# Kernel optimization log

Measured on AMD Instinct MI355X. Metric: run time of the kernel, lower is better.

## Reference

```python
import jax, jax.numpy as jnp
import numpy as np

DIM = 240; NH = 6; HD = 20          # dim, num_heads, head_dim = dim // (2*num_heads)
WS = 16; BWS = 8                    # window size, base window size
R = (WS // BWS) ** 2                # spatial_linear in_features (=4)
LW = WS * WS; LB = BWS * BWS

# static relative-position index for a WSxWS window (same construction as torch buffer)
_coords = np.stack(np.meshgrid(np.arange(WS), np.arange(WS), indexing='ij')).reshape(2, -1)
_rel = (_coords[:, :, None] - _coords[:, None, :]).transpose(1, 2, 0).astype(np.int64)
_rel[..., 0] += WS - 1; _rel[..., 1] += WS - 1; _rel[..., 0] *= 2 * WS - 1
RPI = jnp.asarray(_rel.sum(-1))     # [LW, LW]


def conv2d(x, w, b, pad):
    y = jax.lax.conv_general_dilated(x, w, (1, 1), [(pad, pad), (pad, pad)],
                                     dimension_numbers=('NCHW', 'OIHW', 'NCHW'))
    return y + b[None, :, None, None]


def lrelu(x):
    return jnp.where(x >= 0, x, 0.2 * x)  # LeakyReLU(0.2)


def layer_norm(x, g, b, eps=1e-5):
    m = x.mean(-1, keepdims=True)
    v = jnp.mean((x - m) ** 2, axis=-1, keepdims=True)
    return (x - m) * jax.lax.rsqrt(v + eps) * g + b


def setup_inputs() -> dict:
    key = jax.random.key(0)
    ks = iter(jax.random.split(key, 40))
    rn = lambda shape: jax.random.normal(next(ks), shape, jnp.float32) * 0.02
    B, H, W = 2, 256, 256
    pd = (DIM // 4) // 4  # DynamicPosBias pos_dim = 15
    return {
        'x': jax.random.normal(next(ks), (B, H * W, DIM), jnp.float32),
        # DFE (qv projection)
        'c1_w': rn((DIM // 5, DIM, 1, 1)), 'c1_b': jnp.zeros((DIM // 5,), jnp.float32),
        'c2_w': rn((DIM // 5, DIM // 5, 3, 3)), 'c2_b': jnp.zeros((DIM // 5,), jnp.float32),
        'c3_w': rn((DIM, DIM // 5, 1, 1)), 'c3_b': jnp.zeros((DIM,), jnp.float32),
        'lin_w': rn((DIM, DIM, 1, 1)), 'lin_b': jnp.zeros((DIM,), jnp.float32),
        # spatial linear projection Linear(R, 1)
        'sl_w': rn((1, R)), 'sl_b': jnp.zeros((1,), jnp.float32),
        # DynamicPosBias MLP (residual=False)
        'pp_w': rn((pd, 2)), 'pp_b': jnp.zeros((pd,), jnp.float32),
        'ln1_g': jnp.ones((pd,), jnp.float32), 'ln1_b': jnp.zeros((pd,), jnp.float32),
        'p1_w': rn((pd, pd)), 'p1_b': jnp.zeros((pd,), jnp.float32),
        'ln2_g': jnp.ones((pd,), jnp.float32), 'ln2_b': jnp.zeros((pd,), jnp.float32),
        'p2_w': rn((pd, pd)), 'p2_b': jnp.zeros((pd,), jnp.float32),
        'ln3_g': jnp.ones((pd,), jnp.float32), 'ln3_b': jnp.zeros((pd,), jnp.float32),
        'p3_w': rn((NH, pd)), 'p3_b': jnp.zeros((NH,), jnp.float32),
        # output projection
        'proj_w': rn((DIM, DIM)), 'proj_b': jnp.zeros((DIM,), jnp.float32),
        'H': 256, 'W': 256,
    }


def reference(x, c1_w, c1_b, c2_w, c2_b, c3_w, c3_b, lin_w, lin_b, sl_w, sl_b,
              pp_w, pp_b, ln1_g, ln1_b, p1_w, p1_b, ln2_g, ln2_b, p2_w, p2_b,
              ln3_g, ln3_b, p3_w, p3_b, proj_w, proj_b, H, W):
    B, L, C = x.shape
    # ---- DFE feature projection (conv-gated) ----
    xi = jnp.transpose(x, (0, 2, 1)).reshape(B, C, H, W)
    conv = conv2d(lrelu(conv2d(lrelu(conv2d(xi, c1_w, c1_b, 0)), c2_w, c2_b, 1)), c3_w, c3_b, 0)
    qv = conv * conv2d(xi, lin_w, lin_b, 0)                       # [B,C,H,W]
    qv = jnp.transpose(qv, (0, 2, 3, 1))                          # [B,H,W,C]
    # ---- window partition ----
    nh_w, nw_w = H // WS, W // WS
    qv = qv.reshape(B, nh_w, WS, nw_w, WS, C).transpose(0, 1, 3, 2, 4, 5).reshape(-1, LW, C)
    B_ = qv.shape[0]
    qv = qv.reshape(B_, LW, 2, NH, HD).transpose(2, 0, 3, 1, 4)   # [2,B_,NH,LW,HD]
    q, v = qv[0], qv[1]
    # ---- spatial self-correlation ----
    # spatial linear projection of v: [B_,NH,LW,HD] -> [B_,NH,LB,HD]
    vs = v.reshape(B_, NH, BWS, WS // BWS, BWS, WS // BWS, HD)
    vs = vs.transpose(0, 1, 2, 4, 6, 3, 5).reshape(B_, NH, LB, HD, R)
    vs = jnp.einsum('bnkcr,or->bnkc', vs, sl_w) + sl_b            # Linear(R,1), squeezed
    corr = jnp.einsum('bnlc,bnkc->bnlk', q, vs) / HD              # [B_,NH,LW,LB]
    # dynamic relative position bias (MLP over the mother set of relative coords)
    ph = jnp.arange(1 - WS, WS)
    biases = jnp.stack(jnp.meshgrid(ph, ph, indexing='ij')).reshape(2, -1).T.astype(x.dtype)
    pos = biases @ pp_w.T + pp_b
    pos = jax.nn.relu(layer_norm(pos, ln1_g, ln1_b)) @ p1_w.T + p1_b
    pos = jax.nn.relu(layer_norm(pos, ln2_g, ln2_b)) @ p2_w.T + p2_b
    pos = jax.nn.relu(layer_norm(pos, ln3_g, ln3_b)) @ p3_w.T + p3_b  # [(2*WS-1)^2, NH]
    rpb = jnp.take(pos, RPI.reshape(-1), axis=0).reshape(LW, LW, NH).transpose(2, 0, 1)
    # pool key axis to base-window resolution (consistent with spatial_linear_projection grouping)
    rpb = rpb.reshape(NH, LW, BWS, WS // BWS, BWS, WS // BWS).mean((3, 5)).reshape(NH, LW, LB)
    corr = corr + rpb[None]
    x_s = jnp.einsum('bnlk,bnkc->bnlc', corr, vs)
    x_s = x_s.transpose(0, 2, 1, 3).reshape(B_, LW, NH * HD)      # [B_,LW,C/2]
    # ---- channel self-correlation (single-head over merged channels) ----
    qc = q.transpose(0, 2, 1, 3).reshape(B_, LW, NH * HD)
    vc = v.transpose(0, 2, 1, 3).reshape(B_, LW, NH * HD)
    corr_c = jnp.einsum('blc,bld->bcd', qc, vc) / LW              # [B_,C/2,C/2]
    x_c = jnp.einsum('bcd,bld->blc', corr_c, vc)                  # [B_,LW,C/2]
    # ---- window reverse + spatial-channel fusion ----
    def wrev(t):
        return t.reshape(B, nh_w, nw_w, WS, WS, -1).transpose(0, 1, 3, 2, 4, 5).reshape(B, H, W, -1)
    out = jnp.concatenate([wrev(x_s), wrev(x_c)], axis=-1)        # [B,H,W,C]
    out = out @ proj_w.T + proj_b
    return out.reshape(B, L, C)
```

## Files before the change

### kernel.cpp

```cpp
#include <hip/hip_runtime.h>
#include <math.h>

#define NPIX 131072

typedef __attribute__((ext_vector_type(8))) short bfrag;
typedef __attribute__((ext_vector_type(4))) float facc;
typedef __attribute__((ext_vector_type(4))) unsigned short us4;

__device__ __forceinline__ float lrelu_f(float x) { return x >= 0.f ? x : 0.2f * x; }

__device__ __forceinline__ int pix_of(int w, int l) {
    int b = w >> 8, wi = (w >> 4) & 15, wj = w & 15;
    return ((((b << 4) + wi) * 16 + (l >> 4)) << 8) + (wj << 4) + (l & 15);
}

__device__ __forceinline__ unsigned short bf16rn(float f) {
    unsigned u = __builtin_bit_cast(unsigned, f);
    u += 0x7FFFu + ((u >> 16) & 1u);
    return (unsigned short)(u >> 16);
}
__device__ __forceinline__ float bf16tof(unsigned short h) {
    unsigned u = ((unsigned)h) << 16;
    return __builtin_bit_cast(float, u);
}

__device__ __forceinline__ void split_x_body(const float* __restrict__ x,
                                             unsigned short* __restrict__ xs2, int idx)
{
    int row = idx >> 5;
    int k = (idx & 31) * 8;
    float v[8];
    if (k < 240) {
        float4 a = *(const float4*)(x + (size_t)row * 240 + k);
        float4 b = *(const float4*)(x + (size_t)row * 240 + k + 4);
        v[0] = a.x; v[1] = a.y; v[2] = a.z; v[3] = a.w;
        v[4] = b.x; v[5] = b.y; v[6] = b.z; v[7] = b.w;
    } else {
#pragma unroll
        for (int e = 0; e < 8; ++e) v[e] = 0.f;
    }
    bfrag hi, lo;
#pragma unroll
    for (int e = 0; e < 8; ++e) {
        unsigned short h = bf16rn(v[e]);
        hi[e] = (short)h;
        lo[e] = (short)bf16rn(v[e] - bf16tof(h));
    }
    unsigned short* dst = xs2 + (size_t)row * 512 + k;
    *(bfrag*)(dst) = hi;
    *(bfrag*)(dst + 256) = lo;
}

__device__ __forceinline__ void pack_w_body(const float* __restrict__ src,
                                            int rows, int K,
                                            unsigned short* __restrict__ dst,
                                            int total8, int KPAD, int idx)
{
    if (idx >= total8) return;
    int kper = KPAD >> 3;
    int row = idx / kper;
    int k = (idx - row * kper) * 8;
    float v[8];
#pragma unroll
    for (int e = 0; e < 8; ++e) {
        int kk = k + e;
        v[e] = (row < rows && kk < K) ? src[(size_t)row * K + kk] : 0.f;
    }
    bfrag hi, lo;
#pragma unroll
    for (int e = 0; e < 8; ++e) {
        unsigned short h = bf16rn(v[e]);
        hi[e] = (short)h;
        lo[e] = (short)bf16rn(v[e] - bf16tof(h));
    }
    unsigned short* d = dst + (size_t)row * 2 * KPAD + k;
    *(bfrag*)(d) = hi;
    *(bfrag*)(d + KPAD) = lo;
}

__device__ __forceinline__ void pack_c2w_body(const float* __restrict__ c2_w,
                                              unsigned short* __restrict__ c2w2, int idx)
{
    if (idx >= 6912) return;
    int rowid = idx >> 4;
    int c = idx & 15;
    int tap = rowid / 48, n = rowid - tap * 48;
    int ty = tap / 3, tx = tap - ty * 3;
    int lohalf = c >> 3;
    int cbase = (c & 7) * 8;
    bfrag outv;
#pragma unroll
    for (int e = 0; e < 8; ++e) {
        int ci = cbase + e;
        float v = (ci < 48) ? c2_w[(((size_t)n * 48 + ci) * 3 + ty) * 3 + tx] : 0.f;
        unsigned short h = bf16rn(v);
        outv[e] = (short)(lohalf ? bf16rn(v - bf16tof(h)) : h);
    }
    *(bfrag*)(c2w2 + (size_t)rowid * 128 + c * 8) = outv;
}

__global__ __launch_bounds__(256) void pack_all_kernel(
    const float* __restrict__ lin_w, const float* __restrict__ proj_w,
    const float* __restrict__ c3_w, const float* __restrict__ c1_w,
    const float* __restrict__ c2_w, const float* __restrict__ x,
    unsigned short* __restrict__ lin_w2, unsigned short* __restrict__ proj_w2,
    unsigned short* __restrict__ c3_w2, unsigned short* __restrict__ c1_w2,
    unsigned short* __restrict__ c2w2, unsigned short* __restrict__ xs2)
{
    int blk = blockIdx.x, tid = threadIdx.x;
    if (blk < 32)       pack_w_body(lin_w, 240, 240, lin_w2, 8192, 256, blk * 256 + tid);
    else if (blk < 64)  pack_w_body(proj_w, 240, 240, proj_w2, 8192, 256, (blk - 32) * 256 + tid);
    else if (blk < 72)  pack_w_body(c3_w, 240, 48, c3_w2, 2048, 64, (blk - 64) * 256 + tid);
    else if (blk < 88)  pack_w_body(c1_w, 48, 240, c1_w2, 4096, 256, (blk - 72) * 256 + tid);
    else if (blk < 115) pack_c2w_body(c2_w, c2w2, (blk - 88) * 256 + tid);
    else                split_x_body(x, xs2, (blk - 115) * 256 + tid);
}

__device__ __forceinline__ void ln_relu15(const float* h, float* r,
                                          const float* __restrict__ g,
                                          const float* __restrict__ b) {
    float m = 0.f;
#pragma unroll
    for (int f = 0; f < 15; ++f) m += h[f];
    m *= (1.f / 15.f);
    float v = 0.f;
#pragma unroll
    for (int f = 0; f < 15; ++f) { float d = h[f] - m; v += d * d; }
    float rs = rsqrtf(v * (1.f / 15.f) + 1e-5f);
#pragma unroll
    for (int f = 0; f < 15; ++f) {
        float xx = (h[f] - m) * rs * g[f] + b[f];
        r[f] = xx > 0.f ? xx : 0.f;
    }
}

__device__ __forceinline__ void lin15(const float* r, float* h,
                                      const float* __restrict__ w,
                                      const float* __restrict__ b) {
#pragma unroll
    for (int o = 0; o < 15; ++o) {
        float s = b[o];
#pragma unroll
        for (int g = 0; g < 15; ++g) s += r[g] * w[o * 15 + g];
        h[o] = s;
    }
}

__global__ __launch_bounds__(256) void prep_pos_kernel(
    const float* __restrict__ pp_w, const float* __restrict__ pp_b,
    const float* __restrict__ ln1_g, const float* __restrict__ ln1_b,
    const float* __restrict__ p1_w, const float* __restrict__ p1_b,
    const float* __restrict__ ln2_g, const float* __restrict__ ln2_b,
    const float* __restrict__ p2_w, const float* __restrict__ p2_b,
    const float* __restrict__ ln3_g, const float* __restrict__ ln3_b,
    const float* __restrict__ p3_w, const float* __restrict__ p3_b,
    float* __restrict__ pos3)
{
    int idx = blockIdx.x * 256 + threadIdx.x;
    if (idx >= 961) return;
    float h[15], r[15];
    float in0 = (float)(idx / 31) - 15.f;
    float in1 = (float)(idx % 31) - 15.f;
#pragma unroll
    for (int f = 0; f < 15; ++f) h[f] = in0 * pp_w[2 * f] + in1 * pp_w[2 * f + 1] + pp_b[f];
    ln_relu15(h, r, ln1_g, ln1_b);
    lin15(r, h, p1_w, p1_b);
    ln_relu15(h, r, ln2_g, ln2_b);
    lin15(r, h, p2_w, p2_b);
    ln_relu15(h, r, ln3_g, ln3_b);
#pragma unroll
    for (int o = 0; o < 6; ++o) {
        float s = p3_b[o];
#pragma unroll
        for (int g = 0; g < 15; ++g) s += r[g] * p3_w[o * 15 + g];
        pos3[idx * 6 + o] = s;
    }
}

__global__ __launch_bounds__(256) void rpb_kernel(const float* __restrict__ pos3,
                                                  float* __restrict__ rpb_t)
{
    int out = blockIdx.x * 256 + threadIdx.x;
    int n = out >> 14;
    int k = (out >> 8) & 63;
    int l = out & 255;
    int a = k >> 3, c = k & 7;
    int i1 = l >> 4, j1 = l & 15;
    float s = 0.f;
#pragma unroll
    for (int bb = 0; bb < 2; ++bb)
#pragma unroll
        for (int d = 0; d < 2; ++d) {
            int i2 = a * 2 + bb, j2 = c * 2 + d;
            int rpi = (i1 - i2 + 15) * 31 + (j1 - j2 + 15);
            s += pos3[rpi * 6 + n];
        }
    rpb_t[out] = s * 0.25f;
}

__device__ __forceinline__ void mfma_kpass3(const unsigned short* __restrict__ A2, int lda2,
                                            const unsigned short* __restrict__ W2, int ldw2,
                                            int ksteps, int mbase, int nbase,
                                            short* lds_a, short* lds_w,
                                            int tid, int wm, int wn,
                                            facc acc[4][4])
{
    int lane = tid & 63;
    int i = lane & 15, g = lane >> 4;
    int kpa = lda2 >> 1, kpw = ldw2 >> 1;
    for (int s = 0; s < ksteps; ++s) {
        int k0 = s * 32;
        {
            int r = tid >> 1, h16 = (tid & 1) * 16;
            const unsigned short* src = A2 + (size_t)(mbase + r) * lda2 + k0 + h16;
            bfrag h0 = *(const bfrag*)(src);
            bfrag h1 = *(const bfrag*)(src + 8);
            bfrag l0 = *(const bfrag*)(src + kpa);
            bfrag l1 = *(const bfrag*)(src + kpa + 8);
            short* dst = lds_a + r * 72 + h16;
            *(bfrag*)(dst)      = h0;  *(bfrag*)(dst + 8)  = h1;
            *(bfrag*)(dst + 32) = l0;  *(bfrag*)(dst + 40) = l1;
        }
        {
            int r = tid >> 1, half = tid & 1;
            const unsigned short* src = W2 + (size_t)(nbase + r) * ldw2 + half * kpw + k0;
            bfrag v0 = *(const bfrag*)(src);
            bfrag v1 = *(const bfrag*)(src + 8);
            bfrag v2 = *(const bfrag*)(src + 16);
            bfrag v3 = *(const bfrag*)(src + 24);
            short* dst = lds_w + r * 72 + half * 32;
            *(bfrag*)(dst)      = v0;  *(bfrag*)(dst + 8)  = v1;
            *(bfrag*)(dst + 16) = v2;  *(bfrag*)(dst + 24) = v3;
        }
        __syncthreads();
        bfrag ah[4], al[4], bh[4], bl[4];
#pragma unroll
        for (int mu = 0; mu < 4; ++mu) {
            const short* p = lds_a + (wm * 64 + mu * 16 + i) * 72 + g * 8;
            ah[mu] = *(const bfrag*)(p);
            al[mu] = *(const bfrag*)(p + 32);
        }
#pragma unroll
        for (int nu = 0; nu < 4; ++nu) {
            const short* p = lds_w + (wn * 64 + nu * 16 + i) * 72 + g * 8;
            bh[nu] = *(const bfrag*)(p);
            bl[nu] = *(const bfrag*)(p + 32);
        }
#pragma unroll
        for (int mu = 0; mu < 4; ++mu)
#pragma unroll
            for (int nu = 0; nu < 4; ++nu) {
                acc[mu][nu] = __builtin_amdgcn_mfma_f32_16x16x32_bf16(ah[mu], bh[nu], acc[mu][nu], 0, 0, 0);
                acc[mu][nu] = __builtin_amdgcn_mfma_f32_16x16x32_bf16(ah[mu], bl[nu], acc[mu][nu], 0, 0, 0);
                acc[mu][nu] = __builtin_amdgcn_mfma_f32_16x16x32_bf16(al[mu], bh[nu], acc[mu][nu], 0, 0, 0);
            }
        __syncthreads();
    }
}

__device__ __forceinline__ void mfma_kpass_n64(const unsigned short* __restrict__ A2, int lda2,
                                               const unsigned short* __restrict__ W2, int ldw2,
                                               int ksteps, int mbase,
                                               short* lds_a, short* lds_w,
                                               int tid, int wm, int wn,
                                               facc acc[4][2])
{
    int lane = tid & 63;
    int i = lane & 15, g = lane >> 4;
    int kpa = lda2 >> 1, kpw = ldw2 >> 1;
    for (int s = 0; s < ksteps; ++s) {
        int k0 = s * 32;
        {
            int r = tid >> 1, h16 = (tid & 1) * 16;
            const unsigned short* src = A2 + (size_t)(mbase + r) * lda2 + k0 + h16;
            bfrag h0 = *(const bfrag*)(src);
            bfrag h1 = *(const bfrag*)(src + 8);
            bfrag l0 = *(const bfrag*)(src + kpa);
            bfrag l1 = *(const bfrag*)(src + kpa + 8);
            short* dst = lds_a + r * 72 + h16;
            *(bfrag*)(dst)      = h0;  *(bfrag*)(dst + 8)  = h1;
            *(bfrag*)(dst + 32) = l0;  *(bfrag*)(dst + 40) = l1;
        }
        if (tid < 128) {
            int r = tid >> 1, half = tid & 1;
            const unsigned short* src = W2 + (size_t)r * ldw2 + half * kpw + k0;
            bfrag v0 = *(const bfrag*)(src);
            bfrag v1 = *(const bfrag*)(src + 8);
            bfrag v2 = *(const bfrag*)(src + 16);
            bfrag v3 = *(const bfrag*)(src + 24);
            short* dst = lds_w + r * 72 + half * 32;
            *(bfrag*)(dst)      = v0;  *(bfrag*)(dst + 8)  = v1;
            *(bfrag*)(dst + 16) = v2;  *(bfrag*)(dst + 24) = v3;
        }
        __syncthreads();
        bfrag ah[4], al[4], bh[2], bl[2];
#pragma unroll
        for (int mu = 0; mu < 4; ++mu) {
            const short* p = lds_a + (wm * 64 + mu * 16 + i) * 72 + g * 8;
            ah[mu] = *(const bfrag*)(p);
            al[mu] = *(const bfrag*)(p + 32);
        }
#pragma unroll
        for (int nu = 0; nu < 2; ++nu) {
            const short* p = lds_w + (wn * 32 + nu * 16 + i) * 72 + g * 8;
            bh[nu] = *(const bfrag*)(p);
            bl[nu] = *(const bfrag*)(p + 32);
        }
#pragma unroll
        for (int mu = 0; mu < 4; ++mu)
#pragma unroll
            for (int nu = 0; nu < 2; ++nu) {
                acc[mu][nu] = __builtin_amdgcn_mfma_f32_16x16x32_bf16(ah[mu], bh[nu], acc[mu][nu], 0, 0, 0);
                acc[mu][nu] = __builtin_amdgcn_mfma_f32_16x16x32_bf16(ah[mu], bl[nu], acc[mu][nu], 0, 0, 0);
                acc[mu][nu] = __builtin_amdgcn_mfma_f32_16x16x32_bf16(al[mu], bh[nu], acc[mu][nu], 0, 0, 0);
            }
        __syncthreads();
    }
}

__global__ __launch_bounds__(256, 3) void conv1_mfma_kernel(const unsigned short* __restrict__ xs2,
    const unsigned short* __restrict__ c1_w2, const float* __restrict__ bias,
    unsigned short* __restrict__ t1s)
{
    __shared__ __align__(16) short lds_a[128 * 72];
    __shared__ __align__(16) short lds_w[64 * 72];
    int tid = threadIdx.x;
    int lane = tid & 63, wid = tid >> 6;
    int wm = wid >> 1, wn = wid & 1;
    int mbase = blockIdx.x * 128;
    facc zero = {0.f, 0.f, 0.f, 0.f};
    facc acc[4][2];
#pragma unroll
    for (int mu = 0; mu < 4; ++mu)
#pragma unroll
        for (int nu = 0; nu < 2; ++nu) acc[mu][nu] = zero;

    mfma_kpass_n64(xs2, 512, c1_w2, 512, 8, mbase, lds_a, lds_w, tid, wm, wn, acc);

    int i = lane & 15, g = lane >> 4;
#pragma unroll
    for (int nu = 0; nu < 2; ++nu) {
        int n = wn * 32 + nu * 16 + i;
        if (n < 48) {
            float bv = bias[n];
#pragma unroll
            for (int mu = 0; mu < 4; ++mu)
#pragma unroll
                for (int rr = 0; rr < 4; ++rr) {
                    size_t m = (size_t)mbase + wm * 64 + mu * 16 + g * 4 + rr;
                    float v = lrelu_f(acc[mu][nu][rr] + bv);
                    unsigned short h = bf16rn(v);
                    t1s[m * 128 + n] = h;
                    t1s[m * 128 + 64 + n] = bf16rn(v - bf16tof(h));
                }
        }
    }
    if (tid < 128) {
        size_t m = (size_t)mbase + tid;
        bfrag z = {0, 0, 0, 0, 0, 0, 0, 0};
        *(bfrag*)(t1s + m * 128 + 48)  = z;
        *(bfrag*)(t1s + m * 128 + 56)  = z;
        *(bfrag*)(t1s + m * 128 + 112) = z;
        *(bfrag*)(t1s + m * 128 + 120) = z;
    }
}

__global__ __launch_bounds__(256) void conv2_mfma_kernel(const unsigned short* __restrict__ t1s,
    const unsigned short* __restrict__ c2w2, const float* __restrict__ bias,
    unsigned short* __restrict__ t2s)
{
    __shared__ __align__(16) short a_s[130 * 128];
    int bid = blockIdx.x;
    int xcd = bid & 7;
    int j = bid >> 3;
    int half = j & 1;
    int rl = (j >> 1) & 31;
    int b = j >> 6;
    int r = xcd * 32 + rl;
    int c0 = half * 128;
    int tid = threadIdx.x;
    int lane = tid & 63, wid = tid >> 6;
    int i = lane & 15, g = lane >> 4;
    facc zero = {0.f, 0.f, 0.f, 0.f};
    facc acc[2][3];
#pragma unroll
    for (int mu = 0; mu < 2; ++mu)
#pragma unroll
        for (int nu = 0; nu < 3; ++nu) acc[mu][nu] = zero;

    for (int dy = 0; dy < 3; ++dy) {
        int grow = r + dy - 1;
        bool rowok = (grow >= 0 && grow < 256);
        for (int idx = tid; idx < 130 * 16; idx += 256) {
            int j2 = idx >> 4, ch = idx & 15;
            int gc = c0 - 1 + j2;
            bfrag v = {0, 0, 0, 0, 0, 0, 0, 0};
            if (rowok && gc >= 0 && gc < 256) {
                size_t gpix = ((size_t)b * 256 + grow) * 256 + gc;
                v = *(const bfrag*)(t1s + gpix * 128 + ch * 8);
            }
            *(bfrag*)&a_s[j2 * 128 + ((ch ^ (j2 & 7)) * 8)] = v;
        }
        __syncthreads();
#pragma unroll
        for (int dx = 0; dx < 3; ++dx) {
            const unsigned short* wb = c2w2 + (size_t)(dy * 3 + dx) * 48 * 128;
#pragma unroll
            for (int h = 0; h < 2; ++h) {
                bfrag ah[2], al[2], bh[3], bl[3];
#pragma unroll
                for (int mu = 0; mu < 2; ++mu) {
                    int j2 = wid * 32 + mu * 16 + i + dx;
                    int chi = (h * 4 + g) ^ (j2 & 7);
                    int clo = (8 + h * 4 + g) ^ (j2 & 7);
                    ah[mu] = *(const bfrag*)&a_s[j2 * 128 + chi * 8];
                    al[mu] = *(const bfrag*)&a_s[j2 * 128 + clo * 8];
                }
#pragma unroll
                for (int nu = 0; nu < 3; ++nu) {
                    const unsigned short* wp = wb + (size_t)(nu * 16 + i) * 128 + h * 32 + g * 8;
                    bh[nu] = *(const bfrag*)(wp);
                    bl[nu] = *(const bfrag*)(wp + 64);
                }
#pragma unroll
                for (int mu = 0; mu < 2; ++mu)
#pragma unroll
                    for (int nu = 0; nu < 3; ++nu) {
                        acc[mu][nu] = __builtin_amdgcn_mfma_f32_16x16x32_bf16(ah[mu], bh[nu], acc[mu][nu], 0, 0, 0);
                        acc[mu][nu] = __builtin_amdgcn_mfma_f32_16x16x32_bf16(ah[mu], bl[nu], acc[mu][nu], 0, 0, 0);
                        acc[mu][nu] = __builtin_amdgcn_mfma_f32_16x16x32_bf16(al[mu], bh[nu], acc[mu][nu], 0, 0, 0);
                    }
            }
        }
        __syncthreads();
    }
#pragma unroll
    for (int nu = 0; nu < 3; ++nu) {
        int n = nu * 16 + i;
        float bv = bias[n];
#pragma unroll
        for (int mu = 0; mu < 2; ++mu)
#pragma unroll
            for (int rr = 0; rr < 4; ++rr) {
                int lp = wid * 32 + mu * 16 + g * 4 + rr;
                size_t gpix = ((size_t)b * 256 + r) * 256 + (c0 + lp);
                float v = lrelu_f(acc[mu][nu][rr] + bv);
                unsigned short h = bf16rn(v);
                t2s[gpix * 128 + n] = h;
                t2s[gpix * 128 + 64 + n] = bf16rn(v - bf16tof(h));
            }
    }
    if (tid < 128) {
        size_t gpix = ((size_t)b * 256 + r) * 256 + (c0 + tid);
        bfrag z = {0, 0, 0, 0, 0, 0, 0, 0};
        *(bfrag*)(t2s + gpix * 128 + 48)  = z;
        *(bfrag*)(t2s + gpix * 128 + 56)  = z;
        *(bfrag*)(t2s + gpix * 128 + 112) = z;
        *(bfrag*)(t2s + gpix * 128 + 120) = z;
    }
}

__global__ __launch_bounds__(256) void qv_mfma_kernel(const unsigned short* __restrict__ xs2,
    const unsigned short* __restrict__ lin_w2, const float* __restrict__ lin_b,
    const unsigned short* __restrict__ t2s, const unsigned short* __restrict__ c3_w2,
    const float* __restrict__ c3_b, float* __restrict__ qv)
{
    __shared__ __align__(16) short lds_a[128 * 72];
    __shared__ __align__(16) short lds_w[128 * 72];
    int tid = threadIdx.x;
    int lane = tid & 63, wid = tid >> 6;
    int wm = wid >> 1, wn = wid & 1;
    int bid = blockIdx.y * 2 + blockIdx.x;
    int xcd = bid & 7, j = bid >> 3;
    int mbase = (xcd * 128 + (j >> 1)) * 128;
    int nbase = (j & 1) * 128;
    facc zero = {0.f, 0.f, 0.f, 0.f};
    facc acc1[4][4], acc2[4][4];
#pragma unroll
    for (int mu = 0; mu < 4; ++mu)
#pragma unroll
        for (int nu = 0; nu < 4; ++nu) { acc1[mu][nu] = zero; acc2[mu][nu] = zero; }

    mfma_kpass3(xs2, 512, lin_w2, 512, 8, mbase, nbase, lds_a, lds_w, tid, wm, wn, acc1);
    mfma_kpass3(t2s, 128, c3_w2, 128, 2, mbase, nbase, lds_a, lds_w, tid, wm, wn, acc2);

    int i = lane & 15, g = lane >> 4;
#pragma unroll
    for (int nu = 0; nu < 4; ++nu) {
        int n = nbase + wn * 64 + nu * 16 + i;
        if (n < 240) {
            float lb = lin_b[n], cb = c3_b[n];
#pragma unroll
            for (int mu = 0; mu < 4; ++mu)
#pragma unroll
                for (int rr = 0; rr < 4; ++rr) {
                    size_t m = (size_t)mbase + wm * 64 + mu * 16 + g * 4 + rr;
                    qv[m * 240 + n] = (acc2[mu][nu][rr] + cb) * (acc1[mu][nu][rr] + lb);
                }
        }
    }
}

__global__ __launch_bounds__(256, 3) void proj_mfma_kernel(const unsigned short* __restrict__ cat2,
    const unsigned short* __restrict__ proj_w2, const float* __restrict__ bias,
    float* __restrict__ out)
{
    __shared__ __align__(16) short lds_a[128 * 72];
    __shared__ __align__(16) short lds_w[128 * 72];
    int tid = threadIdx.x;
    int lane = tid & 63, wid = tid >> 6;
    int wm = wid >> 1, wn = wid & 1;
    int bid = blockIdx.y * 2 + blockIdx.x;
    int xcd = bid & 7, j = bid >> 3;
    int mbase = (xcd * 128 + (j >> 1)) * 128;
    int nbase = (j & 1) * 128;
    facc zero = {0.f, 0.f, 0.f, 0.f};
    facc acc[4][4];
#pragma unroll
    for (int mu = 0; mu < 4; ++mu)
#pragma unroll
        for (int nu = 0; nu < 4; ++nu) acc[mu][nu] = zero;

    mfma_kpass3(cat2, 512, proj_w2, 512, 8, mbase, nbase, lds_a, lds_w, tid, wm, wn, acc);

    int i = lane & 15, g = lane >> 4;
#pragma unroll
    for (int nu = 0; nu < 4; ++nu) {
        int n = nbase + wn * 64 + nu * 16 + i;
        if (n < 240) {
            float bv = bias[n];
#pragma unroll
            for (int mu = 0; mu < 4; ++mu)
#pragma unroll
                for (int rr = 0; rr < 4; ++rr) {
                    size_t m = (size_t)mbase + wm * 64 + mu * 16 + g * 4 + rr;
                    out[m * 240 + n] = acc[mu][nu][rr] + bv;
                }
        }
    }
}

__global__ __launch_bounds__(256) void xs_kernel(const float* __restrict__ qv,
    const float* __restrict__ rpb_t, const float* __restrict__ sl_w,
    const float* __restrict__ sl_b, unsigned short* __restrict__ cat2)
{
    __shared__ __align__(16) float v_s[256 * 20];
    __shared__ __align__(16) float vs_s[64 * 20];
    int bid = blockIdx.x;
    int xcd = bid & 7;
    int j = bid >> 3;
    int wl = j / 6;
    int n = j - wl * 6;
    int w = xcd * 64 + wl;
    int tid = threadIdx.x;
    int l = tid;
    size_t pix = (size_t)pix_of(w, l);
    const float* qp = qv + pix * 240 + n * 20;
    float qr[20];
#pragma unroll
    for (int h4 = 0; h4 < 5; ++h4) {
        *(float4*)&qr[h4 * 4] = *(const float4*)(qp + h4 * 4);
        *(float4*)&v_s[l * 20 + h4 * 4] = *(const float4*)(qp + 120 + h4 * 4);
    }
    __syncthreads();
    float slw0 = sl_w[0], slw1 = sl_w[1], slw2 = sl_w[2], slw3 = sl_w[3];
    float slb = sl_b[0];
    for (int idx = tid; idx < 1280; idx += 256) {
        int k = idx / 20, hd = idx % 20;
        int a = k >> 3, c = k & 7;
        int l00 = a * 32 + c * 2;
        float vsum = slb
                   + slw0 * v_s[(l00 + 0) * 20 + hd]
                   + slw1 * v_s[(l00 + 1) * 20 + hd]
                   + slw2 * v_s[(l00 + 16) * 20 + hd]
                   + slw3 * v_s[(l00 + 17) * 20 + hd];
        vs_s[idx] = vsum;
    }
    __syncthreads();
    const float* rp = rpb_t + (size_t)n * 16384 + l;
    float acc[20];
#pragma unroll
    for (int hd = 0; hd < 20; ++hd) acc[hd] = 0.f;
#pragma unroll
    for (int k = 0; k < 64; ++k) {
        float vr[20];
#pragma unroll
        for (int h4 = 0; h4 < 5; ++h4)
            *(float4*)&vr[h4 * 4] = *(const float4*)&vs_s[k * 20 + h4 * 4];
        float s0 = 0.f, s1 = 0.f, s2 = 0.f, s3 = 0.f;
#pragma unroll
        for (int hd = 0; hd < 20; hd += 4) {
            s0 += qr[hd + 0] * vr[hd + 0];
            s1 += qr[hd + 1] * vr[hd + 1];
            s2 += qr[hd + 2] * vr[hd + 2];
            s3 += qr[hd + 3] * vr[hd + 3];
        }
        float cc = (s0 + s1 + s2 + s3) * (1.f / 20.f) + rp[(size_t)k * 256];
#pragma unroll
        for (int hd = 0; hd < 20; ++hd) acc[hd] += cc * vr[hd];
    }
    unsigned short* op = cat2 + pix * 512 + n * 20;
#pragma unroll
    for (int h4 = 0; h4 < 5; ++h4) {
        us4 h, lo;
#pragma unroll
        for (int e = 0; e < 4; ++e) {
            float v = acc[h4 * 4 + e];
            unsigned short hh = bf16rn(v);
            h[e] = hh;
            lo[e] = bf16rn(v - bf16tof(hh));
        }
        *(us4*)(op + h4 * 4) = h;
        *(us4*)(op + 256 + h4 * 4) = lo;
    }
    if (n == 0) {
        bfrag z = {0, 0, 0, 0, 0, 0, 0, 0};
        unsigned short* zp = cat2 + pix * 512;
        *(bfrag*)(zp + 240) = z;  *(bfrag*)(zp + 248) = z;
        *(bfrag*)(zp + 496) = z;  *(bfrag*)(zp + 504) = z;
    }
}

__global__ __launch_bounds__(256) void corrxc_kernel(const float* __restrict__ qv,
                                                     unsigned short* __restrict__ cat2)
{
    __shared__ __align__(16) float G_s[120 * 124];
    __shared__ __align__(16) float vc_s[16 * 124];
    __shared__ __align__(16) float qc_s[16 * 124];
    __shared__ __align__(16) float a_s[8 * 132];
    int bid = blockIdx.x;
    int w = (bid & 7) * 64 + (bid >> 3);
    int tid = threadIdx.x, ty = tid >> 4, tx = tid & 15;

    float acc[8][8] = {};
    for (int l0 = 0; l0 < 256; l0 += 16) {
        for (int idx = tid; idx < 480; idx += 256) {
            int k = idx / 30, c4 = idx % 30;
            size_t pix = (size_t)pix_of(w, l0 + k);
            const float* qp = qv + pix * 240;
            *(float4*)&qc_s[k * 124 + c4 * 4] = *(const float4*)(qp + c4 * 4);
            *(float4*)&vc_s[k * 124 + c4 * 4] = *(const float4*)(qp + 120 + c4 * 4);
        }
        __syncthreads();
#pragma unroll
        for (int k = 0; k < 16; ++k) {
            float4 a0 = *(const float4*)&vc_s[k * 124 + ty * 8];
            float4 a1 = *(const float4*)&vc_s[k * 124 + ty * 8 + 4];
            float4 b0 = *(const float4*)&qc_s[k * 124 + tx * 8];
            float4 b1 = *(const float4*)&qc_s[k * 124 + tx * 8 + 4];
            float av[8] = {a0.x, a0.y, a0.z, a0.w, a1.x, a1.y, a1.z, a1.w};
            float bv[8] = {b0.x, b0.y, b0.z, b0.w, b1.x, b1.y, b1.z, b1.w};
#pragma unroll
            for (int i = 0; i < 8; ++i)
#pragma unroll
                for (int j = 0; j < 8; ++j) acc[i][j] += av[i] * bv[j];
        }
        __syncthreads();
    }
#pragma unroll
    for (int i = 0; i < 8; ++i) {
        int d = ty * 8 + i;
        if (d < 120) {
#pragma unroll
            for (int j4 = 0; j4 < 2; ++j4) {
                int c = tx * 8 + j4 * 4;
                if (c < 120) {
                    float4 o;
                    o.x = acc[i][j4 * 4 + 0]; o.y = acc[i][j4 * 4 + 1];
                    o.z = acc[i][j4 * 4 + 2]; o.w = acc[i][j4 * 4 + 3];
                    *(float4*)&G_s[d * 124 + c] = o;
                }
            }
        }
    }
    __syncthreads();

    for (int mh = 0; mh < 2; ++mh) {
#pragma unroll
        for (int i = 0; i < 8; ++i)
#pragma unroll
            for (int j2 = 0; j2 < 8; ++j2) acc[i][j2] = 0.f;
        for (int k0 = 0; k0 < 120; k0 += 8) {
            {
                int lloc = tid >> 1;
                int kk = (tid & 1) * 4;
                int l = mh * 128 + lloc;
                size_t pix = (size_t)pix_of(w, l);
                float4 v = *(const float4*)(qv + pix * 240 + 120 + k0 + kk);
                a_s[(kk + 0) * 132 + lloc] = v.x;
                a_s[(kk + 1) * 132 + lloc] = v.y;
                a_s[(kk + 2) * 132 + lloc] = v.z;
                a_s[(kk + 3) * 132 + lloc] = v.w;
            }
            __syncthreads();
#pragma unroll
            for (int k = 0; k < 8; ++k) {
                float4 a0 = *(const float4*)&a_s[k * 132 + ty * 8];
                float4 a1 = *(const float4*)&a_s[k * 132 + ty * 8 + 4];
                float4 b0 = *(const float4*)&G_s[(k0 + k) * 124 + tx * 8];
                float4 b1 = *(const float4*)&G_s[(k0 + k) * 124 + tx * 8 + 4];
                float av[8] = {a0.x, a0.y, a0.z, a0.w, a1.x, a1.y, a1.z, a1.w};
                float bv[8] = {b0.x, b0.y, b0.z, b0.w, b1.x, b1.y, b1.z, b1.w};
#pragma unroll
                for (int i = 0; i < 8; ++i)
#pragma unroll
                    for (int j2 = 0; j2 < 8; ++j2) acc[i][j2] += av[i] * bv[j2];
            }
            __syncthreads();
        }
#pragma unroll
        for (int i = 0; i < 8; ++i) {
            int l = mh * 128 + ty * 8 + i;
            size_t pix = (size_t)pix_of(w, l);
            unsigned short* op = cat2 + pix * 512;
#pragma unroll
            for (int j4 = 0; j4 < 2; ++j4) {
                int c = tx * 8 + j4 * 4;
                if (c < 120) {
                    us4 h, lo;
#pragma unroll
                    for (int e = 0; e < 4; ++e) {
                        float v = acc[i][j4 * 4 + e] * (1.f / 256.f);
                        unsigned short hh = bf16rn(v);
                        h[e] = hh;
                        lo[e] = bf16rn(v - bf16tof(hh));
                    }
                    *(us4*)(op + 120 + c) = h;
                    *(us4*)(op + 256 + 120 + c) = lo;
                }
            }
        }
    }
}

extern "C" void kernel_launch(void* const* d_in, const int* in_sizes, int n_in,
                              void* d_out, int out_size, void* d_ws, size_t ws_size,
                              hipStream_t stream)
{
    (void)in_sizes; (void)n_in; (void)out_size;
    const float* x     = (const float*)d_in[0];
    const float* c1_w  = (const float*)d_in[1];
    const float* c1_b  = (const float*)d_in[2];
    const float* c2_w  = (const float*)d_in[3];
    const float* c2_b  = (const float*)d_in[4];
    const float* c3_w  = (const float*)d_in[5];
    const float* c3_b  = (const float*)d_in[6];
    const float* lin_w = (const float*)d_in[7];
    const float* lin_b = (const float*)d_in[8];
    const float* sl_w  = (const float*)d_in[9];
    const float* sl_b  = (const float*)d_in[10];
    const float* pp_w  = (const float*)d_in[11];
    const float* pp_b  = (const float*)d_in[12];
    const float* ln1_g = (const float*)d_in[13];
    const float* ln1_b = (const float*)d_in[14];
    const float* p1_w  = (const float*)d_in[15];
    const float* p1_b  = (const float*)d_in[16];
    const float* ln2_g = (const float*)d_in[17];
    const float* ln2_b = (const float*)d_in[18];
    const float* p2_w  = (const float*)d_in[19];
    const float* p2_b  = (const float*)d_in[20];
    const float* ln3_g = (const float*)d_in[21];
    const float* ln3_b = (const float*)d_in[22];
    const float* p3_w  = (const float*)d_in[23];
    const float* p3_b  = (const float*)d_in[24];
    const float* proj_w = (const float*)d_in[25];
    const float* proj_b = (const float*)d_in[26];

    float* ws = (float*)d_ws;
    float* pos3   = ws;
    float* rpb_t  = ws + 8192;
    unsigned short* lin_w2  = (unsigned short*)(ws + 106496);
    unsigned short* c3_w2   = (unsigned short*)(ws + 172032);
    unsigned short* proj_w2 = (unsigned short*)(ws + 188416);
    unsigned short* c1_w2   = (unsigned short*)(ws + 253952);
    unsigned short* c2w2    = (unsigned short*)(ws + 286720);
    unsigned short* t2s = (unsigned short*)(ws + 314368);
    unsigned short* xs2 = (unsigned short*)(ws + 8702976);
    unsigned short* cat2 = xs2;
    float* qvb    = ws + 42257408;
    unsigned short* t1s = (unsigned short*)qvb;
    const size_t required = (size_t)73714688 * 4;
    if (ws_size < required) return;

    pack_all_kernel<<<16499, 256, 0, stream>>>(lin_w, proj_w, c3_w, c1_w, c2_w, x,
                                               lin_w2, proj_w2, c3_w2, c1_w2, c2w2, xs2);
    prep_pos_kernel<<<4, 256, 0, stream>>>(pp_w, pp_b, ln1_g, ln1_b, p1_w, p1_b,
                                           ln2_g, ln2_b, p2_w, p2_b, ln3_g, ln3_b,
                                           p3_w, p3_b, pos3);
    rpb_kernel<<<384, 256, 0, stream>>>(pos3, rpb_t);
    conv1_mfma_kernel<<<1024, 256, 0, stream>>>(xs2, c1_w2, c1_b, t1s);
    conv2_mfma_kernel<<<1024, 256, 0, stream>>>(t1s, c2w2, c2_b, t2s);
    qv_mfma_kernel<<<dim3(2, 1024), 256, 0, stream>>>(xs2, lin_w2, lin_b, t2s, c3_w2, c3_b, qvb);
    xs_kernel<<<3072, 256, 0, stream>>>(qvb, rpb_t, sl_w, sl_b, cat2);
    corrxc_kernel<<<512, 256, 0, stream>>>(qvb, cat2);
    proj_mfma_kernel<<<dim3(2, 1024), 256, 0, stream>>>(cat2, proj_w2, proj_b, (float*)d_out);
}
```

Before: 542.0 us.

## Move channel-correlation GEMMs in corrxc onto bf16 split-precision MFMA

Rewrites corrxc_kernel so both GEMMs (the Gram matrix qc^T·vc and the product of vc with the Gram matrix) use 16x16x32 bf16 MFMA instead of scalar FP32 FMA outer products. Each FP32 operand is split into hi and lo bf16 parts and three MFMA passes (hi·hi, hi·lo, lo·hi) approximate FP32 accuracy. Operands are staged in LDS as bf16 hi/lo tiles padded to 128 channels, and the Gram matrix is stored transposed in bf16 split form, using about 86 KB of dynamic shared memory. The large LDS footprint lowers occupancy, and the final output writes change from vectorised stores to scalar 16-bit stores.

```diff
diff --git a/kernel.cpp b/kernel.cpp
--- a/kernel.cpp
+++ b/kernel.cpp
@@ -624,109 +624,161 @@
 __global__ __launch_bounds__(256) void corrxc_kernel(const float* __restrict__ qv,
                                                      unsigned short* __restrict__ cat2)
 {
-    __shared__ __align__(16) float G_s[120 * 124];
-    __shared__ __align__(16) float vc_s[16 * 124];
-    __shared__ __align__(16) float qc_s[16 * 124];
-    __shared__ __align__(16) float a_s[8 * 132];
+    extern __shared__ short smem[];
+    short* lds_g = smem;
+    short* ph1_a = smem;
+    short* ph1_w = smem + 9216;
+    short* ph2_a = smem + 33792;
+
     int bid = blockIdx.x;
     int w = (bid & 7) * 64 + (bid >> 3);
-    int tid = threadIdx.x, ty = tid >> 4, tx = tid & 15;
-
-    float acc[8][8] = {};
-    for (int l0 = 0; l0 < 256; l0 += 16) {
-        for (int idx = tid; idx < 480; idx += 256) {
-            int k = idx / 30, c4 = idx % 30;
-            size_t pix = (size_t)pix_of(w, l0 + k);
-            const float* qp = qv + pix * 240;
-            *(float4*)&qc_s[k * 124 + c4 * 4] = *(const float4*)(qp + c4 * 4);
-            *(float4*)&vc_s[k * 124 + c4 * 4] = *(const float4*)(qp + 120 + c4 * 4);
+    int tid = threadIdx.x;
+    int lane = tid & 63, wid = tid >> 6;
+    int wm = wid >> 1, wn = wid & 1;
+    int i = lane & 15, g = lane >> 4;
+    facc zero = {0.f, 0.f, 0.f, 0.f};
+    facc acc[4][4];
+#pragma unroll
+    for (int mu = 0; mu < 4; ++mu)
+#pragma unroll
+        for (int nu = 0; nu < 4; ++nu) acc[mu][nu] = zero;
+
+    for (int l0 = 0; l0 < 256; l0 += 32) {
+        int dl = tid & 31;
+        int ch0 = (tid >> 5) * 16;
+        const float* qp = qv + (size_t)pix_of(w, l0 + dl) * 240;
+#pragma unroll
+        for (int j4 = 0; j4 < 4; ++j4) {
+            int c0 = ch0 + j4 * 4;
+            float4 fa = make_float4(0.f, 0.f, 0.f, 0.f);
+            float4 fb = make_float4(0.f, 0.f, 0.f, 0.f);
+            if (c0 < 120) {
+                fa = *(const float4*)(qp + 120 + c0);
+                fb = *(const float4*)(qp + c0);
+            }
+            float ea[4] = {fa.x, fa.y, fa.z, fa.w};
+            float eb[4] = {fb.x, fb.y, fb.z, fb.w};
+#pragma unroll
+            for (int e = 0; e < 4; ++e) {
+                int ch = c0 + e;
+                unsigned short h = bf16rn(ea[e]);
+                ph1_a[ch * 72 + dl]      = (short)h;
+                ph1_a[ch * 72 + 32 + dl] = (short)bf16rn(ea[e] - bf16tof(h));
+                h = bf16rn(eb[e]);
+                ph1_w[ch * 72 + dl]      = (short)h;
+                ph1_w[ch * 72 + 32 + dl] = (short)bf16rn(eb[e] - bf16tof(h));
+            }
         }
         __syncthreads();
-#pragma unroll
-        for (int k = 0; k < 16; ++k) {
-            float4 a0 = *(const float4*)&vc_s[k * 124 + ty * 8];
-            float4 a1 = *(const float4*)&vc_s[k * 124 + ty * 8 + 4];
-            float4 b0 = *(const float4*)&qc_s[k * 124 + tx * 8];
-            float4 b1 = *(const float4*)&qc_s[k * 124 + tx * 8 + 4];
-            float av[8] = {a0.x, a0.y, a0.z, a0.w, a1.x, a1.y, a1.z, a1.w};
-            float bv[8] = {b0.x, b0.y, b0.z, b0.w, b1.x, b1.y, b1.z, b1.w};
-#pragma unroll
-            for (int i = 0; i < 8; ++i)
-#pragma unroll
-                for (int j = 0; j < 8; ++j) acc[i][j] += av[i] * bv[j];
-        }
+        bfrag ah[4], al2[4], bh[4], bl2[4];
+#pragma unroll
+        for (int mu = 0; mu < 4; ++mu) {
+            const short* p = ph1_a + (wm * 64 + mu * 16 + i) * 72 + g * 8;
+            ah[mu] = *(const bfrag*)(p);
+            al2[mu] = *(const bfrag*)(p + 32);
+        }
+#pragma unroll
+        for (int nu = 0; nu < 4; ++nu) {
+            const short* p = ph1_w + (wn * 64 + nu * 16 + i) * 72 + g * 8;
+            bh[nu] = *(const bfrag*)(p);
+            bl2[nu] = *(const bfrag*)(p + 32);
+        }
+#pragma unroll
+        for (int mu = 0; mu < 4; ++mu)
+#pragma unroll
+            for (int nu = 0; nu < 4; ++nu) {
+                acc[mu][nu] = __builtin_amdgcn_mfma_f32_16x16x32_bf16(ah[mu], bh[nu], acc[mu][nu], 0, 0, 0);
+                acc[mu][nu] = __builtin_amdgcn_mfma_f32_16x16x32_bf16(ah[mu], bl2[nu], acc[mu][nu], 0, 0, 0);
+                acc[mu][nu] = __builtin_amdgcn_mfma_f32_16x16x32_bf16(al2[mu], bh[nu], acc[mu][nu], 0, 0, 0);
+            }
         __syncthreads();
     }
 #pragma unroll
-    for (int i = 0; i < 8; ++i) {
-        int d = ty * 8 + i;
-        if (d < 120) {
-#pragma unroll
-            for (int j4 = 0; j4 < 2; ++j4) {
-                int c = tx * 8 + j4 * 4;
-                if (c < 120) {
-                    float4 o;
-                    o.x = acc[i][j4 * 4 + 0]; o.y = acc[i][j4 * 4 + 1];
-                    o.z = acc[i][j4 * 4 + 2]; o.w = acc[i][j4 * 4 + 3];
-                    *(float4*)&G_s[d * 124 + c] = o;
+    for (int mu = 0; mu < 4; ++mu)
+#pragma unroll
+        for (int nu = 0; nu < 4; ++nu)
+#pragma unroll
+            for (int rr = 0; rr < 4; ++rr) {
+                int d = wm * 64 + mu * 16 + g * 4 + rr;
+                int c = wn * 64 + nu * 16 + i;
+                float v = acc[mu][nu][rr];
+                unsigned short h = bf16rn(v);
+                lds_g[c * 264 + d]       = (short)h;
+                lds_g[c * 264 + 128 + d] = (short)bf16rn(v - bf16tof(h));
+            }
+
+    for (int mh = 0; mh < 2; ++mh) {
+#pragma unroll
+        for (int mu = 0; mu < 4; ++mu)
+#pragma unroll
+            for (int nu = 0; nu < 4; ++nu) acc[mu][nu] = zero;
+        for (int k0 = 0; k0 < 128; k0 += 32) {
+            {
+                int r = tid >> 1, h16 = (tid & 1) * 16;
+                const float* qp = qv + (size_t)pix_of(w, mh * 128 + r) * 240 + 120;
+                float v[16];
+#pragma unroll
+                for (int j4 = 0; j4 < 4; ++j4) {
+                    int d0 = k0 + h16 + j4 * 4;
+                    float4 f = make_float4(0.f, 0.f, 0.f, 0.f);
+                    if (d0 < 120) f = *(const float4*)(qp + d0);
+                    v[j4 * 4 + 0] = f.x; v[j4 * 4 + 1] = f.y;
+                    v[j4 * 4 + 2] = f.z; v[j4 * 4 + 3] = f.w;
                 }
-            }
-        }
-    }
-    __syncthreads();
-
-    for (int mh = 0; mh < 2; ++mh) {
-#pragma unroll
-        for (int i = 0; i < 8; ++i)
-#pragma unroll
-            for (int j2 = 0; j2 < 8; ++j2) acc[i][j2] = 0.f;
-        for (int k0 = 0; k0 < 120; k0 += 8) {
-            {
-                int lloc = tid >> 1;
-                int kk = (tid & 1) * 4;
-                int l = mh * 128 + lloc;
+                bfrag h0, h1, lo0, lo1;
+#pragma unroll
+                for (int e = 0; e < 8; ++e) {
+                    unsigned short h = bf16rn(v[e]);
+                    h0[e] = (short)h;
+                    lo0[e] = (short)bf16rn(v[e] - bf16tof(h));
+                    h = bf16rn(v[8 + e]);
+                    h1[e] = (short)h;
+                    lo1[e] = (short)bf16rn(v[8 + e] - bf16tof(h));
+                }
+                short* dst = ph2_a + r * 72 + h16;
+                *(bfrag*)(dst)      = h0;  *(bfrag*)(dst + 8)  = h1;
+                *(bfrag*)(dst + 32) = lo0; *(bfrag*)(dst + 40) = lo1;
+            }
+            __syncthreads();
+            bfrag ah[4], al2[4], bh[4], bl2[4];
+#pragma unroll
+            for (int mu = 0; mu < 4; ++mu) {
+                const short* p = ph2_a + (wm * 64 + mu * 16 + i) * 72 + g * 8;
+                ah[mu] = *(const bfrag*)(p);
+                al2[mu] = *(const bfrag*)(p + 32);
+            }
+#pragma unroll
+            for (int nu = 0; nu < 4; ++nu) {
+                const short* p = lds_g + (wn * 64 + nu * 16 + i) * 264 + k0 + g * 8;
+                bh[nu] = *(const bfrag*)(p);
+                bl2[nu] = *(const bfrag*)(p + 128);
+            }
+#pragma unroll
+            for (int mu = 0; mu < 4; ++mu)
+#pragma unroll
+                for (int nu = 0; nu < 4; ++nu) {
+                    acc[mu][nu] = __builtin_amdgcn_mfma_f32_16x16x32_bf16(ah[mu], bh[nu], acc[mu][nu], 0, 0, 0);
+                    acc[mu][nu] = __builtin_amdgcn_mfma_f32_16x16x32_bf16(ah[mu], bl2[nu], acc[mu][nu], 0, 0, 0);
+                    acc[mu][nu] = __builtin_amdgcn_mfma_f32_16x16x32_bf16(al2[mu], bh[nu], acc[mu][nu], 0, 0, 0);
+                }
+            __syncthreads();
+        }
+#pragma unroll
+        for (int mu = 0; mu < 4; ++mu) {
+#pragma unroll
+            for (int rr = 0; rr < 4; ++rr) {
+                int l = mh * 128 + wm * 64 + mu * 16 + g * 4 + rr;
                 size_t pix = (size_t)pix_of(w, l);
-                float4 v = *(const float4*)(qv + pix * 240 + 120 + k0 + kk);
-                a_s[(kk + 0) * 132 + lloc] = v.x;
-                a_s[(kk + 1) * 132 + lloc] = v.y;
-                a_s[(kk + 2) * 132 + lloc] = v.z;
-                a_s[(kk + 3) * 132 + lloc] = v.w;
-            }
-            __syncthreads();
-#pragma unroll
-            for (int k = 0; k < 8; ++k) {
-                float4 a0 = *(const float4*)&a_s[k * 132 + ty * 8];
-                float4 a1 = *(const float4*)&a_s[k * 132 + ty * 8 + 4];
-                float4 b0 = *(const float4*)&G_s[(k0 + k) * 124 + tx * 8];
-                float4 b1 = *(const float4*)&G_s[(k0 + k) * 124 + tx * 8 + 4];
-                float av[8] = {a0.x, a0.y, a0.z, a0.w, a1.x, a1.y, a1.z, a1.w};
-                float bv[8] = {b0.x, b0.y, b0.z, b0.w, b1.x, b1.y, b1.z, b1.w};
-#pragma unroll
-                for (int i = 0; i < 8; ++i)
-#pragma unroll
-                    for (int j2 = 0; j2 < 8; ++j2) acc[i][j2] += av[i] * bv[j2];
-            }
-            __syncthreads();
-        }
-#pragma unroll
-        for (int i = 0; i < 8; ++i) {
-            int l = mh * 128 + ty * 8 + i;
-            size_t pix = (size_t)pix_of(w, l);
-            unsigned short* op = cat2 + pix * 512;
-#pragma unroll
-            for (int j4 = 0; j4 < 2; ++j4) {
-                int c = tx * 8 + j4 * 4;
-                if (c < 120) {
-                    us4 h, lo;
-#pragma unroll
-                    for (int e = 0; e < 4; ++e) {
-                        float v = acc[i][j4 * 4 + e] * (1.f / 256.f);
-                        unsigned short hh = bf16rn(v);
-                        h[e] = hh;
-                        lo[e] = bf16rn(v - bf16tof(hh));
+                unsigned short* op = cat2 + pix * 512;
+#pragma unroll
+                for (int nu = 0; nu < 4; ++nu) {
+                    int c = wn * 64 + nu * 16 + i;
+                    if (c < 120) {
+                        float v = acc[mu][nu][rr] * (1.f / 256.f);
+                        unsigned short h = bf16rn(v);
+                        op[120 + c] = h;
+                        op[256 + 120 + c] = bf16rn(v - bf16tof(h));
                     }
-                    *(us4*)(op + 120 + c) = h;
-                    *(us4*)(op + 256 + 120 + c) = lo;
                 }
             }
         }
@@ -792,6 +844,6 @@
     conv2_mfma_kernel<<<1024, 256, 0, stream>>>(t1s, c2w2, c2_b, t2s);
     qv_mfma_kernel<<<dim3(2, 1024), 256, 0, stream>>>(xs2, lin_w2, lin_b, t2s, c3_w2, c3_b, qvb);
     xs_kernel<<<3072, 256, 0, stream>>>(qvb, rpb_t, sl_w, sl_b, cat2);
-    corrxc_kernel<<<512, 256, 0, stream>>>(qvb, cat2);
+    corrxc_kernel<<<512, 256, 86016, stream>>>(qvb, cat2);
     proj_mfma_kernel<<<dim3(2, 1024), 256, 0, stream>>>(cat2, proj_w2, proj_b, (float*)d_out);
 }
```

Result: faster. 508.8 us (median of 2 runs) (-6.1%).
